# Kernel optimization log

Hardware: AMD Instinct MI355X
Metric: run time of the kernel (lower is better)

## Reference

```python
import jax, jax.numpy as jnp
import numpy as np

EPS = 1e-5

def _act_quant(x, bits=8):
    # per-token absmax quantization to signed int range, dequantized (STE)
    qb = float(2 ** (bits - 1) - 1)  # 127 for 8 bits
    scale = qb / jnp.clip(jnp.max(jnp.abs(x), axis=-1, keepdims=True), EPS, None)
    x_dq = jnp.clip(jnp.round(x * scale), -qb, qb) / scale
    return x + jax.lax.stop_gradient(x_dq - x)

def _weight_quant(w):
    # BitNet b1.58 ternary weights: scale = mean |W|, values in {-1,0,1} * scale (STE)
    s = jnp.clip(jnp.mean(jnp.abs(w)), EPS, None)
    w_dq = jnp.clip(jnp.round(w / s), -1.0, 1.0) * s
    return w + jax.lax.stop_gradient(w_dq - w)

def _bitlinear(x, w, bits=8):
    # x: [..., in], w: [out, in]
    return jnp.einsum('bsi,oi->bso', _act_quant(x, bits), _weight_quant(w))

def setup_inputs() -> dict:
    key = jax.random.key(0)
    k1, k2, k3 = jax.random.split(key, 3)
    B, S, H = 4, 4096, 2048
    I = int(H * 2.0)
    return {
        'hidden_states': jax.random.normal(k1, (B, S, H), dtype=jnp.float32),
        'w_up': jax.random.normal(k2, (I, H), dtype=jnp.float32) * (1.0 / np.sqrt(H)),
        'w_down': jax.random.normal(k3, (H, I), dtype=jnp.float32) * (1.0 / np.sqrt(I)),
    }

def reference(hidden_states, w_up, w_down):
    bits = 8
    h = _bitlinear(hidden_states, w_up, bits)          # [B,S,I]
    h = jnp.square(jax.nn.relu(h))                      # squared ReLU
    # dropout p=0.0 (eval) -> identity
    out = _bitlinear(h, w_down, bits)                   # [B,S,H]
    return out
```

## Files before the change

kernel.cpp:

```cpp
#include <hip/hip_runtime.h>
#include <hip/hip_bf16.h>

typedef signed char i8_t;
typedef _Float16 half_t;
typedef float v4fl __attribute__((ext_vector_type(4)));
typedef _Float16 v8h __attribute__((ext_vector_type(8)));
typedef int v4i __attribute__((ext_vector_type(4)));
typedef signed char v8c __attribute__((ext_vector_type(8)));
typedef signed char v16c __attribute__((ext_vector_type(16)));

__device__ __forceinline__ float ternqf(float w, float s) {
    float q = rintf(w / s);
    return fminf(1.f, fmaxf(-1.f, q));
}

__device__ __forceinline__ void gload16(const void* g, void* l) {
    __builtin_amdgcn_global_load_lds(
        (const __attribute__((address_space(1))) void*)g,
        (__attribute__((address_space(3))) void*)l, 16, 0, 0);
}

__global__ void abssum_partial(const float* __restrict__ w, long n,
                               float* __restrict__ partial) {
    long i0 = ((long)blockIdx.x * 256 + threadIdx.x) * 8;
    long stride = (long)gridDim.x * 256 * 8;
    float s = 0.f;
    for (long i = i0; i < n; i += stride) {
        v4fl a = *(const v4fl*)(w + i);
        v4fl b = *(const v4fl*)(w + i + 4);
#pragma unroll
        for (int j = 0; j < 4; ++j) s += fabsf(a[j]) + fabsf(b[j]);
    }
#pragma unroll
    for (int off = 32; off > 0; off >>= 1) s += __shfl_down(s, off, 64);
    __shared__ __align__(16) float red[4];
    if ((threadIdx.x & 63) == 0) red[threadIdx.x >> 6] = s;
    __syncthreads();
    if (threadIdx.x == 0)
        partial[blockIdx.x] = (red[0] + red[1]) + (red[2] + red[3]);
}

__global__ void abssum_final(const float* __restrict__ part_up,
                             const float* __restrict__ part_dn,
                             float* __restrict__ scales, float inv) {
    const int wv = threadIdx.x >> 6;
    const int l = threadIdx.x & 63;
    const float* part = wv ? part_dn : part_up;
    float s = ((part[l] + part[l + 64]) + (part[l + 128] + part[l + 192]));
#pragma unroll
    for (int off = 32; off > 0; off >>= 1) s += __shfl_down(s, off, 64);
    if (l == 0) scales[wv] = fmaxf(s * inv, 1e-5f);
}

__global__ void wquant_kernel(const float* __restrict__ w, i8_t* __restrict__ wq,
                              const float* __restrict__ scale) {
    float s = scale[0];
    long i = ((long)blockIdx.x * 256 + threadIdx.x) * 8;
    v4fl a = *(const v4fl*)(w + i);
    v4fl b = *(const v4fl*)(w + i + 4);
    v8c o;
#pragma unroll
    for (int j = 0; j < 4; ++j) {
        o[j]     = (i8_t)(int)ternqf(a[j], s);
        o[j + 4] = (i8_t)(int)ternqf(b[j], s);
    }
    *(v8c*)(wq + i) = o;
}

__global__ void aquant_kernel(const float* __restrict__ src, i8_t* __restrict__ dst,
                              float* __restrict__ scale_out) {
    const int row = blockIdx.x;
    const int tid = threadIdx.x;
    const float* p = src + (size_t)row * 2048;
    float v[8];
    {
        v4fl a = *(const v4fl*)(p + tid * 8);
        v4fl b = *(const v4fl*)(p + tid * 8 + 4);
#pragma unroll
        for (int j = 0; j < 4; ++j) { v[j] = a[j]; v[j + 4] = b[j]; }
    }
    float amax = 0.f;
#pragma unroll
    for (int j = 0; j < 8; ++j) amax = fmaxf(amax, fabsf(v[j]));
#pragma unroll
    for (int off = 32; off > 0; off >>= 1) amax = fmaxf(amax, __shfl_xor(amax, off, 64));
    __shared__ __align__(16) float red[4];
    __shared__ float bsc;
    if ((tid & 63) == 0) red[tid >> 6] = amax;
    __syncthreads();
    if (tid == 0) {
        float m = fmaxf(fmaxf(red[0], red[1]), fmaxf(red[2], red[3]));
        m = fmaxf(m, 1e-5f);
        scale_out[row] = m / 127.f;
        bsc = 127.f / m;
    }
    __syncthreads();
    float sc = bsc;
    v8c o;
#pragma unroll
    for (int j = 0; j < 8; ++j) {
        float t = rintf(v[j] * sc);
        o[j] = (i8_t)(int)fminf(127.f, fmaxf(-127.f, t));
    }
    *(v8c*)(dst + (size_t)row * 2048 + tid * 8) = o;
}

template <int NV>
__global__ void hquant_kernel(const float* __restrict__ h, i8_t* __restrict__ hq,
                              float* __restrict__ scale_out) {
    const int row = blockIdx.x;
    const int tid = threadIdx.x;
    const int W = NV * 2048;
    const float* p = h + (size_t)row * W + tid * (NV * 8);
    float v[NV * 8];
#pragma unroll
    for (int it = 0; it < NV * 2; ++it) {
        v4fl a = *(const v4fl*)(p + it * 4);
#pragma unroll
        for (int j = 0; j < 4; ++j) v[it * 4 + j] = a[j];
    }
    float amax = 0.f;
#pragma unroll
    for (int j = 0; j < NV * 8; ++j) amax = fmaxf(amax, fabsf(v[j]));
#pragma unroll
    for (int off = 32; off > 0; off >>= 1) amax = fmaxf(amax, __shfl_xor(amax, off, 64));
    __shared__ __align__(16) float red[4];
    __shared__ float bsc;
    if ((tid & 63) == 0) red[tid >> 6] = amax;
    __syncthreads();
    if (tid == 0) {
        float m = fmaxf(fmaxf(red[0], red[1]), fmaxf(red[2], red[3]));
        m = fmaxf(m, 1e-5f);
        scale_out[row] = m / 127.f;
        bsc = 127.f / m;
    }
    __syncthreads();
    const float sc = bsc;
    i8_t* dst = hq + (size_t)row * W + tid * (NV * 8);
    v16c o;
#pragma unroll
    for (int j = 0; j < NV * 8; ++j) {
        float t = rintf(v[j] * sc);
        o[j] = (i8_t)(int)fminf(127.f, fmaxf(-127.f, t));
    }
    *(v16c*)dst = o;
}

template <typename T, int NV>
__global__ void hamax_kernel(const T* __restrict__ h, float* __restrict__ scale_out,
                             float* __restrict__ recip_out) {
    const int row = blockIdx.x;
    const int tid = threadIdx.x;
    const T* p = h + (size_t)row * (NV * 2048);
    float amax = 0.f;
#pragma unroll
    for (int it = 0; it < NV; ++it) {
        const T* s = p + ((size_t)it * 256 + tid) * 8;
#pragma unroll
        for (int j = 0; j < 8; ++j) amax = fmaxf(amax, fabsf((float)s[j]));
    }
#pragma unroll
    for (int off = 32; off > 0; off >>= 1) amax = fmaxf(amax, __shfl_xor(amax, off, 64));
    __shared__ __align__(16) float red[4];
    if ((tid & 63) == 0) red[tid >> 6] = amax;
    __syncthreads();
    if (tid == 0) {
        float m = fmaxf(fmaxf(red[0], red[1]), fmaxf(red[2], red[3]));
        m = fmaxf(m, 1e-5f);
        scale_out[row] = m / 127.f;
        recip_out[row] = 127.f / m;
    }
}

__device__ __forceinline__ void stage_tile256(const i8_t* __restrict__ g, int K,
                                              i8_t* l, int tid) {
#pragma unroll
    for (int i = 0; i < 4; ++i) {
        const int c = i * 512 + tid;
        const int r = c >> 3;
        const int lc = (((c & 7) ^ (r & 7)) << 4);
        gload16(g + (size_t)r * K + lc, l + c * 16);
    }
}

#define MIDBAR() do { \
    __builtin_amdgcn_s_barrier(); \
    __builtin_amdgcn_sched_barrier(0); \
    asm volatile("s_waitcnt lgkmcnt(0)" ::: "memory"); \
    __builtin_amdgcn_sched_barrier(0); } while (0)

#define ENDBAR() do { \
    __builtin_amdgcn_sched_barrier(0); \
    __builtin_amdgcn_s_barrier(); \
    __builtin_amdgcn_sched_barrier(0); } while (0)

template <int EPI>
__launch_bounds__(512, 2)
__global__ void gemm_bt8(const i8_t* __restrict__ A, const i8_t* __restrict__ B,
                         void* __restrict__ Cv,
                         const float* __restrict__ rowscale,
                         const float* __restrict__ wscale,
                         int M, int N, int K) {
    __shared__ __align__(16) i8_t smem[131072];

    const int tid = threadIdx.x;

    const int gx = gridDim.x;
    const int nwg = gx * gridDim.y;
    int flat = blockIdx.y * gx + blockIdx.x;
    if ((nwg & 7) == 0) flat = (flat & 7) * (nwg >> 3) + (flat >> 3);
    const int n0 = (flat % gx) * 256;
    const int m0 = (flat / gx) * 256;

    const i8_t* gA = A + (size_t)m0 * K;
    const i8_t* gB = B + (size_t)n0 * K;

    const int w = tid >> 6, l = tid & 63;
    const int wr = w >> 2, wc = w & 3;
    const int lrow = l & 15, lq = l >> 4;
    const int swz = (lrow & 7) << 4;
    const int c0 = (lq << 4) ^ swz;
    const int aoff0 = ((wr * 128 + lrow) << 7) + c0;
    const int boff0 = ((wc * 64 + lrow) << 7) + c0;

    v4i acc[8][4];
#pragma unroll
    for (int a = 0; a < 8; ++a)
#pragma unroll
        for (int b = 0; b < 4; ++b) acc[a][b] = (v4i){0, 0, 0, 0};

    const int NT = K >> 7;
    stage_tile256(gB, K, smem + 32768, tid);
    stage_tile256(gA, K, smem, tid);
    stage_tile256(gB + 128, K, smem + 65536 + 32768, tid);
    stage_tile256(gA + 128, K, smem + 65536, tid);
    asm volatile("s_waitcnt vmcnt(8)" ::: "memory");
    __builtin_amdgcn_s_barrier();
    __builtin_amdgcn_sched_barrier(0);

    for (int t = 0; t < NT; ++t) {
        i8_t* Ab = smem + ((t & 1) << 16);
        i8_t* Bb = Ab + 32768;
        const bool pf = (t + 2 < NT);

        v4i af[8], bf[4][2];
#pragma unroll
        for (int nj = 0; nj < 4; ++nj) {
            bf[nj][0] = *(const v4i*)(Bb + (boff0 + (nj << 11)));
            bf[nj][1] = *(const v4i*)(Bb + ((boff0 + (nj << 11)) ^ 64));
        }
#pragma unroll
        for (int mi = 0; mi < 8; ++mi)
            af[mi] = *(const v4i*)(Ab + (aoff0 + (mi << 11)));
        MIDBAR();
        __builtin_amdgcn_s_setprio(1);
#pragma unroll
        for (int mi = 0; mi < 8; ++mi)
#pragma unroll
            for (int nj = 0; nj < 2; ++nj)
                acc[mi][nj] = __builtin_amdgcn_mfma_i32_16x16x64_i8(
                    af[mi], bf[nj][0], acc[mi][nj], 0, 0, 0);
        __builtin_amdgcn_s_setprio(0);
        ENDBAR();

        if (pf) stage_tile256(gB + (size_t)(t + 2) * 128, K, Bb, tid);
        MIDBAR();
        __builtin_amdgcn_s_setprio(1);
#pragma unroll
        for (int mi = 0; mi < 8; ++mi)
#pragma unroll
            for (int nj = 2; nj < 4; ++nj)
                acc[mi][nj] = __builtin_amdgcn_mfma_i32_16x16x64_i8(
                    af[mi], bf[nj][0], acc[mi][nj], 0, 0, 0);
        __builtin_amdgcn_s_setprio(0);
        ENDBAR();

#pragma unroll
        for (int mi = 0; mi < 8; ++mi)
            af[mi] = *(const v4i*)(Ab + ((aoff0 + (mi << 11)) ^ 64));
        MIDBAR();
        __builtin_amdgcn_s_setprio(1);
#pragma unroll
        for (int mi = 0; mi < 8; ++mi)
#pragma unroll
            for (int nj = 0; nj < 2; ++nj)
                acc[mi][nj] = __builtin_amdgcn_mfma_i32_16x16x64_i8(
                    af[mi], bf[nj][1], acc[mi][nj], 0, 0, 0);
        __builtin_amdgcn_s_setprio(0);
        ENDBAR();

        if (pf) stage_tile256(gA + (size_t)(t + 2) * 128, K, Ab, tid);
        MIDBAR();
        __builtin_amdgcn_s_setprio(1);
#pragma unroll
        for (int mi = 0; mi < 8; ++mi)
#pragma unroll
            for (int nj = 2; nj < 4; ++nj)
                acc[mi][nj] = __builtin_amdgcn_mfma_i32_16x16x64_i8(
                    af[mi], bf[nj][1], acc[mi][nj], 0, 0, 0);
        __builtin_amdgcn_s_setprio(0);
        __builtin_amdgcn_sched_barrier(0);
        if (pf) {
            asm volatile("s_waitcnt vmcnt(8)" ::: "memory");
        } else if (t + 1 < NT) {
            asm volatile("s_waitcnt vmcnt(0)" ::: "memory");
        }
        if (t + 1 < NT) {
            __builtin_amdgcn_s_barrier();
            __builtin_amdgcn_sched_barrier(0);
        }
    }

    const float sw = wscale[0];
#pragma unroll
    for (int mi = 0; mi < 8; ++mi) {
#pragma unroll
        for (int r = 0; r < 4; ++r) {
            const int row = m0 + wr * 128 + mi * 16 + lq * 4 + r;
            const float rs = sw * rowscale[row];
#pragma unroll
            for (int nj = 0; nj < 4; ++nj) {
                const int col = n0 + wc * 64 + nj * 16 + lrow;
                float v = (float)acc[mi][nj][r] * rs;
                if (EPI == 0) {
                    ((float*)Cv)[(size_t)row * N + col] = v;
                } else {
                    v = fmaxf(v, 0.f); v = v * v;
                    ((float*)Cv)[(size_t)row * N + col] = v;
                }
            }
        }
    }
}

template <int ASRC, int EPI>
__launch_bounds__(256, 2)
__global__ void gemm_bt(const void* __restrict__ Av, const i8_t* __restrict__ B,
                        void* __restrict__ Cv,
                        const float* __restrict__ rowscale,
                        const float* __restrict__ arecip,
                        const float* __restrict__ wscale,
                        int M, int N, int K) {
    __shared__ __align__(16) i8_t As[128 * 64];
    __shared__ __align__(16) i8_t Bs[128 * 64];

    const int tid = threadIdx.x;
    const int gx = gridDim.x;
    const int nwg = gx * gridDim.y;
    int flat = blockIdx.y * gx + blockIdx.x;
    if ((nwg & 7) == 0) flat = (flat & 7) * (nwg >> 3) + (flat >> 3);
    const int n0 = (flat % gx) * 128;
    const int m0 = (flat / gx) * 128;

    const int srow = tid >> 2;
    const int scol = (tid & 3) * 16;
    const i8_t* gB0 = B + (size_t)(n0 + srow) * K + scol;
    const i8_t* gB1 = B + (size_t)(n0 + 64 + srow) * K + scol;
    i8_t* lB0 = Bs + tid * 16;
    i8_t* lB1 = Bs + 4096 + tid * 16;

    const i8_t* gA0 = nullptr;
    const i8_t* gA1 = nullptr;
    i8_t* lA0 = As + tid * 16;
    i8_t* lA1 = As + 4096 + tid * 16;
    if (ASRC == 0) {
        gA0 = (const i8_t*)Av + (size_t)(m0 + srow) * K + scol;
        gA1 = (const i8_t*)Av + (size_t)(m0 + 64 + srow) * K + scol;
    }

    const int qrow = tid >> 1;
    const int qcol = (tid & 1) * 32;
    const float* gA32 = (const float*)Av + (size_t)(m0 + qrow) * K + qcol;
    const half_t* gAh = (const half_t*)Av + (size_t)(m0 + qrow) * K + qcol;
    i8_t* qdst = As + qrow * 64 + qcol;
    const float qsc = (ASRC != 0) ? arecip[m0 + qrow] : 0.f;

    const int w = tid >> 6, l = tid & 63;
    const int wr = w >> 1, wc = w & 1;
    const int lrow = l & 15, lq = l >> 4;

    v4i acc[4][4];
#pragma unroll
    for (int a = 0; a < 4; ++a)
#pragma unroll
        for (int b = 0; b < 4; ++b) acc[a][b] = (v4i){0, 0, 0, 0};

    const int kiters = K / 64;
    for (int kt = 0; kt < kiters; ++kt) {
        const int off = kt * 64;
        v16c r0, r1;
        if (ASRC == 1) {
#pragma unroll
            for (int c = 0; c < 4; ++c) {
                v4fl f0 = *(const v4fl*)(gA32 + off + c * 4);
                v4fl f1 = *(const v4fl*)(gA32 + off + 16 + c * 4);
#pragma unroll
                for (int e = 0; e < 4; ++e) {
                    float t0 = rintf(f0[e] * qsc);
                    float t1 = rintf(f1[e] * qsc);
                    r0[c * 4 + e] = (i8_t)(int)fminf(127.f, fmaxf(-127.f, t0));
                    r1[c * 4 + e] = (i8_t)(int)fminf(127.f, fmaxf(-127.f, t1));
                }
            }
        } else if (ASRC == 2) {
#pragma unroll
            for (int c = 0; c < 2; ++c) {
                v8h h0 = *(const v8h*)(gAh + off + c * 8);
                v8h h1 = *(const v8h*)(gAh + off + 16 + c * 8);
#pragma unroll
                for (int e = 0; e < 8; ++e) {
                    float t0 = rintf((float)h0[e] * qsc);
                    float t1 = rintf((float)h1[e] * qsc);
                    r0[c * 8 + e] = (i8_t)(int)fminf(127.f, fmaxf(-127.f, t0));
                    r1[c * 8 + e] = (i8_t)(int)fminf(127.f, fmaxf(-127.f, t1));
                }
            }
        }
        __syncthreads();
        gload16(gB0 + off, lB0);
        gload16(gB1 + off, lB1);
        if (ASRC == 0) {
            gload16(gA0 + off, lA0);
            gload16(gA1 + off, lA1);
        } else {
            *(v16c*)qdst = r0;
            *(v16c*)(qdst + 16) = r1;
        }
        __syncthreads();

        v4i af[4], bfr[4];
#pragma unroll
        for (int mi = 0; mi < 4; ++mi)
            af[mi] = *(const v4i*)(As + (wr * 64 + mi * 16 + lrow) * 64 + lq * 16);
#pragma unroll
        for (int nj = 0; nj < 4; ++nj)
            bfr[nj] = *(const v4i*)(Bs + (wc * 64 + nj * 16 + lrow) * 64 + lq * 16);
#pragma unroll
        for (int mi = 0; mi < 4; ++mi)
#pragma unroll
            for (int nj = 0; nj < 4; ++nj)
                acc[mi][nj] = __builtin_amdgcn_mfma_i32_16x16x64_i8(
                    af[mi], bfr[nj], acc[mi][nj], 0, 0, 0);
    }

    const float sw = wscale[0];
#pragma unroll
    for (int mi = 0; mi < 4; ++mi) {
#pragma unroll
        for (int r = 0; r < 4; ++r) {
            const int row = m0 + wr * 64 + mi * 16 + lq * 4 + r;
            const float rs = sw * rowscale[row];
#pragma unroll
            for (int nj = 0; nj < 4; ++nj) {
                const int col = n0 + wc * 64 + nj * 16 + lrow;
                float v = (float)acc[mi][nj][r] * rs;
                if (EPI == 0) {
                    ((float*)Cv)[(size_t)row * N + col] = v;
                } else if (EPI == 1) {
                    v = fmaxf(v, 0.f); v = v * v;
                    ((half_t*)Cv)[(size_t)row * N + col] = (half_t)v;
                } else {
                    v = fmaxf(v, 0.f); v = v * v;
                    ((float*)Cv)[(size_t)row * N + col] = v;
                }
            }
        }
    }
}

extern "C" void kernel_launch(void* const* d_in, const int* in_sizes, int n_in,
                              void* d_out, int out_size, void* d_ws, size_t ws_size,
                              hipStream_t stream) {
    const float* x   = (const float*)d_in[0];
    const float* wup = (const float*)d_in[1];
    const float* wdn = (const float*)d_in[2];

    const int H = 2048;
    const int T = in_sizes[0] / H;
    const int I = in_sizes[1] / H;
    const long nw = (long)in_sizes[1];
    const float winv = 1.0f / (float)nw;

    char* p = (char*)d_ws;
    float* scales  = (float*)p;
    float* part_up = (float*)(p + 256);
    float* part_dn = (float*)(p + 1280);
    float* a_scale = (float*)(p + 2304);
    float* h_scale = a_scale + T;
    float* h_recip = h_scale + T;
    size_t off = 2304 + (size_t)12 * T;
    off = (off + 255) & ~(size_t)255;
    i8_t* xq  = (i8_t*)(p + off); off += (size_t)T * H;
    off = (off + 255) & ~(size_t)255;
    i8_t* wqu = (i8_t*)(p + off); off += (size_t)I * H;
    off = (off + 255) & ~(size_t)255;
    i8_t* wqd = (i8_t*)(p + off); off += (size_t)H * I;
    off = (off + 255) & ~(size_t)255;
    void* h  = (void*)(p + off);
    i8_t* hq = (i8_t*)(p + off + (size_t)T * I * 4);

    const size_t need_full = off + (size_t)T * I * 5;
    const size_t need_h32  = off + (size_t)T * I * 4;
    const int mode = (ws_size == 0 || need_full <= ws_size) ? 0
                   : (need_h32 <= ws_size ? 1 : 2);
    const bool big_ok = (T % 256 == 0) && (I % 256 == 0) && (H % 256 == 0) &&
                        (H >= 256) && (I >= 256);

    abssum_partial<<<256, 256, 0, stream>>>(wup, nw, part_up);
    abssum_partial<<<256, 256, 0, stream>>>(wdn, nw, part_dn);
    abssum_final<<<1, 128, 0, stream>>>(part_up, part_dn, scales, winv);

    int wblocks = (int)(nw / 2048);
    wquant_kernel<<<wblocks, 256, 0, stream>>>(wup, wqu, scales + 0);
    wquant_kernel<<<wblocks, 256, 0, stream>>>(wdn, wqd, scales + 1);

    aquant_kernel<<<T, 256, 0, stream>>>(x, xq, a_scale);

    if (mode == 0 && big_ok) {
        gemm_bt8<2><<<dim3(I / 256, T / 256), 512, 0, stream>>>(
            xq, wqu, h, a_scale, scales + 0, T, I, H);
        hquant_kernel<2><<<T, 256, 0, stream>>>((const float*)h, hq, h_scale);
        gemm_bt8<0><<<dim3(H / 256, T / 256), 512, 0, stream>>>(
            hq, wqd, d_out, h_scale, scales + 1, T, H, I);
    } else if (mode == 0) {
        gemm_bt<0, 2><<<dim3(I / 128, T / 128), 256, 0, stream>>>(
            xq, wqu, h, a_scale, nullptr, scales + 0, T, I, H);
        hquant_kernel<2><<<T, 256, 0, stream>>>((const float*)h, hq, h_scale);
        gemm_bt<0, 0><<<dim3(H / 128, T / 128), 256, 0, stream>>>(
            hq, wqd, d_out, h_scale, nullptr, scales + 1, T, H, I);
    } else if (mode == 1) {
        gemm_bt<0, 2><<<dim3(I / 128, T / 128), 256, 0, stream>>>(
            xq, wqu, h, a_scale, nullptr, scales + 0, T, I, H);
        hamax_kernel<float, 2><<<T, 256, 0, stream>>>((const float*)h, h_scale, h_recip);
        gemm_bt<1, 0><<<dim3(H / 128, T / 128), 256, 0, stream>>>(
            h, wqd, d_out, h_scale, h_recip, scales + 1, T, H, I);
    } else {
        gemm_bt<0, 1><<<dim3(I / 128, T / 128), 256, 0, stream>>>(
            xq, wqu, h, a_scale, nullptr, scales + 0, T, I, H);
        hamax_kernel<half_t, 2><<<T, 256, 0, stream>>>((const half_t*)h, h_scale, h_recip);
        gemm_bt<2, 0><<<dim3(H / 128, T / 128), 256, 0, stream>>>(
            h, wqd, d_out, h_scale, h_recip, scales + 1, T, H, I);
    }
}
```

Baseline: 628.8 us.

## Switch int8 GEMM to 32x32x32 MFMA tiles with regrouped LDS fragment loads

Replaces the 16x16x64 int8 MFMA micro-tiling with 32x32x32 int8 MFMAs, so each wave holds a 4x2 grid of 16-wide accumulators instead of an 8x4 grid of 4-wide ones. LDS fragment loads are regrouped per k-slice with recomputed XOR-swizzled offsets, which cuts the number of LDS reads per MFMA. Both next-tile prefetches (A and B) are now issued together in the last phase instead of being spread across phases. The epilogue row mapping changes to match the 32x32 accumulator layout. This risks different register pressure and less overlap between global prefetch and compute.

```diff
diff --git a/kernel.cpp b/kernel.cpp
--- a/kernel.cpp
+++ b/kernel.cpp
@@ -6,6 +6,7 @@
 typedef float v4fl __attribute__((ext_vector_type(4)));
 typedef _Float16 v8h __attribute__((ext_vector_type(8)));
 typedef int v4i __attribute__((ext_vector_type(4)));
+typedef int v16i __attribute__((ext_vector_type(16)));
 typedef signed char v8c __attribute__((ext_vector_type(8)));
 typedef signed char v16c __attribute__((ext_vector_type(16)));
 
@@ -217,17 +218,23 @@
 
     const int w = tid >> 6, l = tid & 63;
     const int wr = w >> 2, wc = w & 3;
-    const int lrow = l & 15, lq = l >> 4;
-    const int swz = (lrow & 7) << 4;
-    const int c0 = (lq << 4) ^ swz;
-    const int aoff0 = ((wr * 128 + lrow) << 7) + c0;
-    const int boff0 = ((wc * 64 + lrow) << 7) + c0;
-
-    v4i acc[8][4];
-#pragma unroll
-    for (int a = 0; a < 8; ++a)
-#pragma unroll
-        for (int b = 0; b < 4; ++b) acc[a][b] = (v4i){0, 0, 0, 0};
+    const int lrow = l & 31;
+    const int lk = l >> 5;
+
+    int kk[4];
+#pragma unroll
+    for (int ks = 0; ks < 4; ++ks)
+        kk[ks] = (((ks * 2 + lk) ^ (lrow & 7)) << 4);
+    const int aBase = (wr * 128 + lrow) << 7;
+    const int bBase = (wc * 64 + lrow) << 7;
+
+    v16i acc[4][2];
+#pragma unroll
+    for (int a = 0; a < 4; ++a)
+#pragma unroll
+        for (int b = 0; b < 2; ++b)
+#pragma unroll
+            for (int e = 0; e < 16; ++e) acc[a][b][e] = 0;
 
     const int NT = K >> 7;
     stage_tile256(gB, K, smem + 32768, tid);
@@ -243,61 +250,75 @@
         i8_t* Bb = Ab + 32768;
         const bool pf = (t + 2 < NT);
 
-        v4i af[8], bf[4][2];
-#pragma unroll
-        for (int nj = 0; nj < 4; ++nj) {
-            bf[nj][0] = *(const v4i*)(Bb + (boff0 + (nj << 11)));
-            bf[nj][1] = *(const v4i*)(Bb + ((boff0 + (nj << 11)) ^ 64));
-        }
-#pragma unroll
-        for (int mi = 0; mi < 8; ++mi)
-            af[mi] = *(const v4i*)(Ab + (aoff0 + (mi << 11)));
+        v4i af[4][4];
+        v4i bf[2][4];
+
+#pragma unroll
+        for (int mi = 0; mi < 4; ++mi)
+            af[0][mi] = *(const v4i*)(Ab + aBase + (mi << 12) + kk[0]);
+#pragma unroll
+        for (int nj = 0; nj < 2; ++nj) {
+            bf[nj][0] = *(const v4i*)(Bb + bBase + (nj << 12) + kk[0]);
+            bf[nj][1] = *(const v4i*)(Bb + bBase + (nj << 12) + kk[1]);
+        }
         MIDBAR();
         __builtin_amdgcn_s_setprio(1);
 #pragma unroll
-        for (int mi = 0; mi < 8; ++mi)
+        for (int mi = 0; mi < 4; ++mi)
 #pragma unroll
             for (int nj = 0; nj < 2; ++nj)
-                acc[mi][nj] = __builtin_amdgcn_mfma_i32_16x16x64_i8(
-                    af[mi], bf[nj][0], acc[mi][nj], 0, 0, 0);
+                acc[mi][nj] = __builtin_amdgcn_mfma_i32_32x32x32_i8(
+                    af[0][mi], bf[nj][0], acc[mi][nj], 0, 0, 0);
         __builtin_amdgcn_s_setprio(0);
         ENDBAR();
 
-        if (pf) stage_tile256(gB + (size_t)(t + 2) * 128, K, Bb, tid);
+#pragma unroll
+        for (int mi = 0; mi < 4; ++mi)
+            af[1][mi] = *(const v4i*)(Ab + aBase + (mi << 12) + kk[1]);
+#pragma unroll
+        for (int nj = 0; nj < 2; ++nj) {
+            bf[nj][2] = *(const v4i*)(Bb + bBase + (nj << 12) + kk[2]);
+            bf[nj][3] = *(const v4i*)(Bb + bBase + (nj << 12) + kk[3]);
+        }
         MIDBAR();
         __builtin_amdgcn_s_setprio(1);
 #pragma unroll
-        for (int mi = 0; mi < 8; ++mi)
-#pragma unroll
-            for (int nj = 2; nj < 4; ++nj)
-                acc[mi][nj] = __builtin_amdgcn_mfma_i32_16x16x64_i8(
-                    af[mi], bf[nj][0], acc[mi][nj], 0, 0, 0);
+        for (int mi = 0; mi < 4; ++mi)
+#pragma unroll
+            for (int nj = 0; nj < 2; ++nj)
+                acc[mi][nj] = __builtin_amdgcn_mfma_i32_32x32x32_i8(
+                    af[1][mi], bf[nj][1], acc[mi][nj], 0, 0, 0);
         __builtin_amdgcn_s_setprio(0);
         ENDBAR();
 
 #pragma unroll
-        for (int mi = 0; mi < 8; ++mi)
-            af[mi] = *(const v4i*)(Ab + ((aoff0 + (mi << 11)) ^ 64));
+        for (int mi = 0; mi < 4; ++mi) {
+            af[2][mi] = *(const v4i*)(Ab + aBase + (mi << 12) + kk[2]);
+            af[3][mi] = *(const v4i*)(Ab + aBase + (mi << 12) + kk[3]);
+        }
         MIDBAR();
         __builtin_amdgcn_s_setprio(1);
 #pragma unroll
-        for (int mi = 0; mi < 8; ++mi)
+        for (int mi = 0; mi < 4; ++mi)
 #pragma unroll
             for (int nj = 0; nj < 2; ++nj)
-                acc[mi][nj] = __builtin_amdgcn_mfma_i32_16x16x64_i8(
-                    af[mi], bf[nj][1], acc[mi][nj], 0, 0, 0);
+                acc[mi][nj] = __builtin_amdgcn_mfma_i32_32x32x32_i8(
+                    af[2][mi], bf[nj][2], acc[mi][nj], 0, 0, 0);
         __builtin_amdgcn_s_setprio(0);
         ENDBAR();
 
-        if (pf) stage_tile256(gA + (size_t)(t + 2) * 128, K, Ab, tid);
+        if (pf) {
+            stage_tile256(gB + (size_t)(t + 2) * 128, K, Bb, tid);
+            stage_tile256(gA + (size_t)(t + 2) * 128, K, Ab, tid);
+        }
         MIDBAR();
         __builtin_amdgcn_s_setprio(1);
 #pragma unroll
-        for (int mi = 0; mi < 8; ++mi)
-#pragma unroll
-            for (int nj = 2; nj < 4; ++nj)
-                acc[mi][nj] = __builtin_amdgcn_mfma_i32_16x16x64_i8(
-                    af[mi], bf[nj][1], acc[mi][nj], 0, 0, 0);
+        for (int mi = 0; mi < 4; ++mi)
+#pragma unroll
+            for (int nj = 0; nj < 2; ++nj)
+                acc[mi][nj] = __builtin_amdgcn_mfma_i32_32x32x32_i8(
+                    af[3][mi], bf[nj][3], acc[mi][nj], 0, 0, 0);
         __builtin_amdgcn_s_setprio(0);
         __builtin_amdgcn_sched_barrier(0);
         if (pf) {
@@ -313,14 +334,14 @@
 
     const float sw = wscale[0];
 #pragma unroll
-    for (int mi = 0; mi < 8; ++mi) {
-#pragma unroll
-        for (int r = 0; r < 4; ++r) {
-            const int row = m0 + wr * 128 + mi * 16 + lq * 4 + r;
+    for (int mi = 0; mi < 4; ++mi) {
+#pragma unroll
+        for (int r = 0; r < 16; ++r) {
+            const int row = m0 + wr * 128 + mi * 32 + (r & 3) + 8 * (r >> 2) + 4 * lk;
             const float rs = sw * rowscale[row];
 #pragma unroll
-            for (int nj = 0; nj < 4; ++nj) {
-                const int col = n0 + wc * 64 + nj * 16 + lrow;
+            for (int nj = 0; nj < 2; ++nj) {
+                const int col = n0 + wc * 64 + nj * 32 + lrow;
                 float v = (float)acc[mi][nj][r] * rs;
                 if (EPI == 0) {
                     ((float*)Cv)[(size_t)row * N + col] = v;
```

Result: slower. 675.8 us (+7.5%).

## Use 1024-thread blocks with K=64 tiles and 64x64 per-wave int8 GEMM

Applied to the files above, without the earlier changes.

Reworks the int8 GEMM so each 256x256 tile is computed by 16 waves instead of 8. Each wave now owns a 64x64 output (4x4 accumulators) and the K step per iteration drops from 128 to 64, which halves LDS to 64KB with a new swizzle. Fewer barrier phases per iteration and smaller register footprint aim for more occupancy and latency hiding. The cost is more barriers per unit of K and less MFMA work between loads per wave. Launch bounds of (1024,4) may not be satisfiable and could force register spills.

```diff
diff --git a/kernel.cpp b/kernel.cpp
--- a/kernel.cpp
+++ b/kernel.cpp
@@ -172,36 +172,31 @@
     }
 }
 
-__device__ __forceinline__ void stage_tile256(const i8_t* __restrict__ g, int K,
-                                              i8_t* l, int tid) {
-#pragma unroll
-    for (int i = 0; i < 4; ++i) {
-        const int c = i * 512 + tid;
-        const int r = c >> 3;
-        const int lc = (((c & 7) ^ (r & 7)) << 4);
-        gload16(g + (size_t)r * K + lc, l + c * 16);
-    }
+__device__ __forceinline__ void stage_tile64(const i8_t* __restrict__ g, int K,
+                                             i8_t* l, int tid) {
+    const int r = tid >> 2;
+    const int s = tid & 3;
+    const int gc = ((s ^ ((r >> 1) & 3)) << 4);
+    gload16(g + (size_t)r * K + gc, l + tid * 16);
 }
 
 #define MIDBAR() do { \
     __builtin_amdgcn_s_barrier(); \
-    __builtin_amdgcn_sched_barrier(0); \
     asm volatile("s_waitcnt lgkmcnt(0)" ::: "memory"); \
     __builtin_amdgcn_sched_barrier(0); } while (0)
 
 #define ENDBAR() do { \
     __builtin_amdgcn_sched_barrier(0); \
-    __builtin_amdgcn_s_barrier(); \
-    __builtin_amdgcn_sched_barrier(0); } while (0)
+    __builtin_amdgcn_s_barrier(); } while (0)
 
 template <int EPI>
-__launch_bounds__(512, 2)
+__launch_bounds__(1024, 4)
 __global__ void gemm_bt8(const i8_t* __restrict__ A, const i8_t* __restrict__ B,
                          void* __restrict__ Cv,
                          const float* __restrict__ rowscale,
                          const float* __restrict__ wscale,
                          int M, int N, int K) {
-    __shared__ __align__(16) i8_t smem[131072];
+    __shared__ __align__(16) i8_t smem[65536];
 
     const int tid = threadIdx.x;
 
@@ -218,105 +213,76 @@
     const int w = tid >> 6, l = tid & 63;
     const int wr = w >> 2, wc = w & 3;
     const int lrow = l & 15, lq = l >> 4;
-    const int swz = (lrow & 7) << 4;
-    const int c0 = (lq << 4) ^ swz;
-    const int aoff0 = ((wr * 128 + lrow) << 7) + c0;
-    const int boff0 = ((wc * 64 + lrow) << 7) + c0;
-
-    v4i acc[8][4];
-#pragma unroll
-    for (int a = 0; a < 8; ++a)
+    const int koff = ((lq ^ ((lrow >> 1) & 3)) << 4);
+    const int aBase = ((wr * 64 + lrow) << 6) + koff;
+    const int bBase = ((wc * 64 + lrow) << 6) + koff;
+
+    v4i acc[4][4];
+#pragma unroll
+    for (int a = 0; a < 4; ++a)
 #pragma unroll
         for (int b = 0; b < 4; ++b) acc[a][b] = (v4i){0, 0, 0, 0};
 
-    const int NT = K >> 7;
-    stage_tile256(gB, K, smem + 32768, tid);
-    stage_tile256(gA, K, smem, tid);
-    stage_tile256(gB + 128, K, smem + 65536 + 32768, tid);
-    stage_tile256(gA + 128, K, smem + 65536, tid);
-    asm volatile("s_waitcnt vmcnt(8)" ::: "memory");
+    const int NT = K >> 6;
+    stage_tile64(gB, K, smem + 16384, tid);
+    stage_tile64(gA, K, smem, tid);
+    stage_tile64(gB + 64, K, smem + 32768 + 16384, tid);
+    stage_tile64(gA + 64, K, smem + 32768, tid);
+    asm volatile("s_waitcnt vmcnt(2)" ::: "memory");
     __builtin_amdgcn_s_barrier();
-    __builtin_amdgcn_sched_barrier(0);
 
     for (int t = 0; t < NT; ++t) {
-        i8_t* Ab = smem + ((t & 1) << 16);
-        i8_t* Bb = Ab + 32768;
+        i8_t* Ab = smem + ((t & 1) << 15);
+        i8_t* Bb = Ab + 16384;
         const bool pf = (t + 2 < NT);
 
-        v4i af[8], bf[4][2];
-#pragma unroll
-        for (int nj = 0; nj < 4; ++nj) {
-            bf[nj][0] = *(const v4i*)(Bb + (boff0 + (nj << 11)));
-            bf[nj][1] = *(const v4i*)(Bb + ((boff0 + (nj << 11)) ^ 64));
-        }
-#pragma unroll
-        for (int mi = 0; mi < 8; ++mi)
-            af[mi] = *(const v4i*)(Ab + (aoff0 + (mi << 11)));
+        v4i af[4], bf[4];
+#pragma unroll
+        for (int mi = 0; mi < 4; ++mi)
+            af[mi] = *(const v4i*)(Ab + aBase + (mi << 10));
+#pragma unroll
+        for (int nj = 0; nj < 4; ++nj)
+            bf[nj] = *(const v4i*)(Bb + bBase + (nj << 10));
         MIDBAR();
         __builtin_amdgcn_s_setprio(1);
 #pragma unroll
-        for (int mi = 0; mi < 8; ++mi)
-#pragma unroll
-            for (int nj = 0; nj < 2; ++nj)
+        for (int mi = 0; mi < 2; ++mi)
+#pragma unroll
+            for (int nj = 0; nj < 4; ++nj)
                 acc[mi][nj] = __builtin_amdgcn_mfma_i32_16x16x64_i8(
-                    af[mi], bf[nj][0], acc[mi][nj], 0, 0, 0);
+                    af[mi], bf[nj], acc[mi][nj], 0, 0, 0);
         __builtin_amdgcn_s_setprio(0);
         ENDBAR();
 
-        if (pf) stage_tile256(gB + (size_t)(t + 2) * 128, K, Bb, tid);
-        MIDBAR();
+        if (pf) {
+            stage_tile64(gB + (size_t)(t + 2) * 64, K, Bb, tid);
+            stage_tile64(gA + (size_t)(t + 2) * 64, K, Ab, tid);
+        }
         __builtin_amdgcn_s_setprio(1);
 #pragma unroll
-        for (int mi = 0; mi < 8; ++mi)
-#pragma unroll
-            for (int nj = 2; nj < 4; ++nj)
+        for (int mi = 2; mi < 4; ++mi)
+#pragma unroll
+            for (int nj = 0; nj < 4; ++nj)
                 acc[mi][nj] = __builtin_amdgcn_mfma_i32_16x16x64_i8(
-                    af[mi], bf[nj][0], acc[mi][nj], 0, 0, 0);
-        __builtin_amdgcn_s_setprio(0);
-        ENDBAR();
-
-#pragma unroll
-        for (int mi = 0; mi < 8; ++mi)
-            af[mi] = *(const v4i*)(Ab + ((aoff0 + (mi << 11)) ^ 64));
-        MIDBAR();
-        __builtin_amdgcn_s_setprio(1);
-#pragma unroll
-        for (int mi = 0; mi < 8; ++mi)
-#pragma unroll
-            for (int nj = 0; nj < 2; ++nj)
-                acc[mi][nj] = __builtin_amdgcn_mfma_i32_16x16x64_i8(
-                    af[mi], bf[nj][1], acc[mi][nj], 0, 0, 0);
-        __builtin_amdgcn_s_setprio(0);
-        ENDBAR();
-
-        if (pf) stage_tile256(gA + (size_t)(t + 2) * 128, K, Ab, tid);
-        MIDBAR();
-        __builtin_amdgcn_s_setprio(1);
-#pragma unroll
-        for (int mi = 0; mi < 8; ++mi)
-#pragma unroll
-            for (int nj = 2; nj < 4; ++nj)
-                acc[mi][nj] = __builtin_amdgcn_mfma_i32_16x16x64_i8(
-                    af[mi], bf[nj][1], acc[mi][nj], 0, 0, 0);
+                    af[mi], bf[nj], acc[mi][nj], 0, 0, 0);
         __builtin_amdgcn_s_setprio(0);
         __builtin_amdgcn_sched_barrier(0);
         if (pf) {
-            asm volatile("s_waitcnt vmcnt(8)" ::: "memory");
+            asm volatile("s_waitcnt vmcnt(2)" ::: "memory");
         } else if (t + 1 < NT) {
             asm volatile("s_waitcnt vmcnt(0)" ::: "memory");
         }
         if (t + 1 < NT) {
             __builtin_amdgcn_s_barrier();
-            __builtin_amdgcn_sched_barrier(0);
         }
     }
 
     const float sw = wscale[0];
 #pragma unroll
-    for (int mi = 0; mi < 8; ++mi) {
+    for (int mi = 0; mi < 4; ++mi) {
 #pragma unroll
         for (int r = 0; r < 4; ++r) {
-            const int row = m0 + wr * 128 + mi * 16 + lq * 4 + r;
+            const int row = m0 + wr * 64 + mi * 16 + lq * 4 + r;
             const float rs = sw * rowscale[row];
 #pragma unroll
             for (int nj = 0; nj < 4; ++nj) {
@@ -517,10 +483,10 @@
     aquant_kernel<<<T, 256, 0, stream>>>(x, xq, a_scale);
 
     if (mode == 0 && big_ok) {
-        gemm_bt8<2><<<dim3(I / 256, T / 256), 512, 0, stream>>>(
+        gemm_bt8<2><<<dim3(I / 256, T / 256), 1024, 0, stream>>>(
             xq, wqu, h, a_scale, scales + 0, T, I, H);
         hquant_kernel<2><<<T, 256, 0, stream>>>((const float*)h, hq, h_scale);
-        gemm_bt8<0><<<dim3(H / 256, T / 256), 512, 0, stream>>>(
+        gemm_bt8<0><<<dim3(H / 256, T / 256), 1024, 0, stream>>>(
             hq, wqd, d_out, h_scale, scales + 1, T, H, I);
     } else if (mode == 0) {
         gemm_bt<0, 2><<<dim3(I / 128, T / 128), 256, 0, stream>>>(
```

New measurement: 662.2 us. 5.3% more time.

## Restructure int8 GEMM inner loop into 4x4 MFMA quadrants with split fragment loads

Applied to the files above, without the earlier changes.

Reorganizes each K-step into four 4x4 MFMA blocks, one per M-half and K-half, instead of 8x2 blocks over N-halves. A and B fragments are now loaded per quadrant with explicit swizzled k offsets, which lowers peak fragment registers and interleaves LDS reads with compute. Both global-to-LDS prefetches move into the last phase, so staging into the current buffer happens only after every read of it is done. In exchange, fewer MFMAs now cover the LDS and staging latency issued in the middle of the step.

```diff
diff --git a/kernel.cpp b/kernel.cpp
--- a/kernel.cpp
+++ b/kernel.cpp
@@ -218,10 +218,11 @@
     const int w = tid >> 6, l = tid & 63;
     const int wr = w >> 2, wc = w & 3;
     const int lrow = l & 15, lq = l >> 4;
-    const int swz = (lrow & 7) << 4;
-    const int c0 = (lq << 4) ^ swz;
-    const int aoff0 = ((wr * 128 + lrow) << 7) + c0;
-    const int boff0 = ((wc * 64 + lrow) << 7) + c0;
+    const int lr7 = lrow & 7;
+    const int kk0 = ((lq)     ^ lr7) << 4;
+    const int kk1 = ((lq + 4) ^ lr7) << 4;
+    const int aBase = ((wr * 128 + lrow) << 7);
+    const int bBase = ((wc * 64 + lrow) << 7);
 
     v4i acc[8][4];
 #pragma unroll
@@ -243,61 +244,71 @@
         i8_t* Bb = Ab + 32768;
         const bool pf = (t + 2 < NT);
 
-        v4i af[8], bf[4][2];
-#pragma unroll
-        for (int nj = 0; nj < 4; ++nj) {
-            bf[nj][0] = *(const v4i*)(Bb + (boff0 + (nj << 11)));
-            bf[nj][1] = *(const v4i*)(Bb + ((boff0 + (nj << 11)) ^ 64));
-        }
-#pragma unroll
-        for (int mi = 0; mi < 8; ++mi)
-            af[mi] = *(const v4i*)(Ab + (aoff0 + (mi << 11)));
+        v4i a0[4], a1[4], b0[4], b1[4];
+
+#pragma unroll
+        for (int mi = 0; mi < 4; ++mi)
+            a0[mi] = *(const v4i*)(Ab + aBase + (mi << 11) + kk0);
+#pragma unroll
+        for (int nj = 0; nj < 4; ++nj)
+            b0[nj] = *(const v4i*)(Bb + bBase + (nj << 11) + kk0);
         MIDBAR();
         __builtin_amdgcn_s_setprio(1);
 #pragma unroll
-        for (int mi = 0; mi < 8; ++mi)
-#pragma unroll
-            for (int nj = 0; nj < 2; ++nj)
+        for (int mi = 0; mi < 4; ++mi)
+#pragma unroll
+            for (int nj = 0; nj < 4; ++nj)
                 acc[mi][nj] = __builtin_amdgcn_mfma_i32_16x16x64_i8(
-                    af[mi], bf[nj][0], acc[mi][nj], 0, 0, 0);
+                    a0[mi], b0[nj], acc[mi][nj], 0, 0, 0);
         __builtin_amdgcn_s_setprio(0);
         ENDBAR();
 
-        if (pf) stage_tile256(gB + (size_t)(t + 2) * 128, K, Bb, tid);
+#pragma unroll
+        for (int mi = 0; mi < 4; ++mi)
+            a1[mi] = *(const v4i*)(Ab + aBase + ((mi + 4) << 11) + kk0);
+#pragma unroll
+        for (int nj = 0; nj < 4; ++nj)
+            b1[nj] = *(const v4i*)(Bb + bBase + (nj << 11) + kk1);
         MIDBAR();
         __builtin_amdgcn_s_setprio(1);
 #pragma unroll
-        for (int mi = 0; mi < 8; ++mi)
-#pragma unroll
-            for (int nj = 2; nj < 4; ++nj)
-                acc[mi][nj] = __builtin_amdgcn_mfma_i32_16x16x64_i8(
-                    af[mi], bf[nj][0], acc[mi][nj], 0, 0, 0);
+        for (int mi = 0; mi < 4; ++mi)
+#pragma unroll
+            for (int nj = 0; nj < 4; ++nj)
+                acc[mi + 4][nj] = __builtin_amdgcn_mfma_i32_16x16x64_i8(
+                    a1[mi], b0[nj], acc[mi + 4][nj], 0, 0, 0);
         __builtin_amdgcn_s_setprio(0);
         ENDBAR();
 
 #pragma unroll
-        for (int mi = 0; mi < 8; ++mi)
-            af[mi] = *(const v4i*)(Ab + ((aoff0 + (mi << 11)) ^ 64));
+        for (int mi = 0; mi < 4; ++mi)
+            a0[mi] = *(const v4i*)(Ab + aBase + (mi << 11) + kk1);
+#pragma unroll
+        for (int mi = 0; mi < 4; ++mi)
+            a1[mi] = *(const v4i*)(Ab + aBase + ((mi + 4) << 11) + kk1);
         MIDBAR();
         __builtin_amdgcn_s_setprio(1);
 #pragma unroll
-        for (int mi = 0; mi < 8; ++mi)
-#pragma unroll
-            for (int nj = 0; nj < 2; ++nj)
+        for (int mi = 0; mi < 4; ++mi)
+#pragma unroll
+            for (int nj = 0; nj < 4; ++nj)
                 acc[mi][nj] = __builtin_amdgcn_mfma_i32_16x16x64_i8(
-                    af[mi], bf[nj][1], acc[mi][nj], 0, 0, 0);
+                    a0[mi], b1[nj], acc[mi][nj], 0, 0, 0);
         __builtin_amdgcn_s_setprio(0);
         ENDBAR();
 
-        if (pf) stage_tile256(gA + (size_t)(t + 2) * 128, K, Ab, tid);
+        if (pf) {
+            stage_tile256(gB + (size_t)(t + 2) * 128, K, Bb, tid);
+            stage_tile256(gA + (size_t)(t + 2) * 128, K, Ab, tid);
+        }
         MIDBAR();
         __builtin_amdgcn_s_setprio(1);
 #pragma unroll
-        for (int mi = 0; mi < 8; ++mi)
-#pragma unroll
-            for (int nj = 2; nj < 4; ++nj)
-                acc[mi][nj] = __builtin_amdgcn_mfma_i32_16x16x64_i8(
-                    af[mi], bf[nj][1], acc[mi][nj], 0, 0, 0);
+        for (int mi = 0; mi < 4; ++mi)
+#pragma unroll
+            for (int nj = 0; nj < 4; ++nj)
+                acc[mi + 4][nj] = __builtin_amdgcn_mfma_i32_16x16x64_i8(
+                    a1[mi], b1[nj], acc[mi + 4][nj], 0, 0, 0);
         __builtin_amdgcn_s_setprio(0);
         __builtin_amdgcn_sched_barrier(0);
         if (pf) {
```

Measured after the change: 647.8 us. 3.0% more time.
